# Kernel tuning notes

Measured on AMD Instinct MI355X. Metric: run time of the kernel, lower is better.

## Reference

```python
import jax, jax.numpy as jnp
import numpy as np

B, C, K, N = 16, 512, 64, 8192
STAGE_NUM = 3


def setup_inputs() -> dict:
    key = jax.random.key(0)
    k0, k1, k2, k3 = jax.random.split(key, 4)
    x = jax.random.normal(k0, (B, C, N), jnp.float32)
    # conv1: Conv1d(c, c, 1) with bias; weight init N(0, sqrt(2/c))
    w1 = jax.random.normal(k1, (C, C), jnp.float32) * np.float32(np.sqrt(2.0 / C))
    b1 = jnp.zeros((C,), jnp.float32)
    # conv2: Conv1d(c, c, 1, bias=False) + BatchNorm1d(c) (gamma=1, beta=0)
    w2 = jax.random.normal(k2, (C, C), jnp.float32) * np.float32(np.sqrt(2.0 / C))
    gamma = jnp.ones((C,), jnp.float32)
    beta = jnp.zeros((C,), jnp.float32)
    # mu buffer: (1, c, k), N(0, sqrt(2/k)); is_normalized=False so no l2norm
    mu0 = jax.random.normal(k3, (1, C, K), jnp.float32) * np.float32(np.sqrt(2.0 / K))
    return {"x": x, "w1": w1, "b1": b1, "mu0": mu0, "w2": w2, "gamma": gamma, "beta": beta}


def reference(x, w1, b1, mu0, w2, gamma, beta):
    idn = x                                             # B,C,N
    # conv1 (1x1 conv == per-point matmul)
    x1 = jnp.einsum('oc,bcn->bon', w1, x) + b1[None, :, None]
    # EM iterations run under torch.no_grad() -> stop_gradient
    xs = jax.lax.stop_gradient(x1)
    mu = jnp.broadcast_to(mu0, (x.shape[0], C, K))      # B,C,K (buffer, no grad)
    z = None
    for _ in range(STAGE_NUM):
        z = jax.nn.softmax(jnp.einsum('bcn,bck->bnk', xs, mu), axis=2)  # E-step
        z_ = z / (1e-6 + z.sum(axis=1, keepdims=True))                  # normalize over N
        mu = jnp.einsum('bcn,bnk->bck', xs, z_)                         # M-step
        # is_normalized=False -> _l2norm is identity
    # reconstruction: mu @ z^T, relu
    x2 = jax.nn.relu(jnp.einsum('bck,bnk->bcn', mu, z))
    # conv2 (1x1, no bias) + BatchNorm1d (training-mode batch stats, eps=1e-5)
    x3 = jnp.einsum('oc,bcn->bon', w2, x2)
    mean = x3.mean(axis=(0, 2), keepdims=True)
    var = x3.var(axis=(0, 2), keepdims=True)
    y = gamma[None, :, None] * (x3 - mean) * jax.lax.rsqrt(var + 1e-5) + beta[None, :, None]
    out = y + idn
    return (out, mu)
```

## Files before the change

### kernel.cpp

```cpp
#include <hip/hip_runtime.h>
#include <math.h>

constexpr int B_ = 16, C_ = 512, K_ = 64, N_ = 8192;
constexpr int BHALF = 8;

typedef __bf16 bf16;
typedef __bf16 bf16x4 __attribute__((ext_vector_type(4)));
typedef __bf16 bf16x8 __attribute__((ext_vector_type(8)));
typedef float f32x4 __attribute__((ext_vector_type(4)));

#define GLDS16(gp, lp)                                              \
  __builtin_amdgcn_global_load_lds(                                 \
      (const __attribute__((address_space(1))) unsigned int*)(gp),  \
      (__attribute__((address_space(3))) unsigned int*)(lp), 16, 0, 0)

__device__ __forceinline__ bf16 lo_part(float v, bf16 h) {
  return (bf16)(v - (float)h);
}

__global__ __launch_bounds__(256) void transpose_split_x(
    const float* __restrict__ X, bf16* __restrict__ XTH, bf16* __restrict__ XTL) {
  const int b = blockIdx.z, c0 = blockIdx.y * 64, n0 = blockIdx.x * 64;
  __shared__ float tile[64][65];
  const int tid = threadIdx.x;
  const int rr = tid >> 4, q4 = (tid & 15) << 2;
#pragma unroll
  for (int r = 0; r < 4; ++r) {
    const int c = r * 16 + rr;
    *reinterpret_cast<float4*>(&tile[c][q4]) = *reinterpret_cast<const float4*>(
        &X[((size_t)b * C_ + c0 + c) * N_ + n0 + q4]);
  }
  __syncthreads();
#pragma unroll
  for (int r = 0; r < 4; ++r) {
    const int n = r * 16 + rr;
    bf16x4 oh, ol;
#pragma unroll
    for (int e = 0; e < 4; ++e) {
      const float v = tile[q4 + e][n];
      const bf16 h = (bf16)v;
      oh[e] = h;
      ol[e] = lo_part(v, h);
    }
    const size_t off = ((size_t)b * N_ + n0 + n) * C_ + c0 + q4;
    *reinterpret_cast<bf16x4*>(&XTH[off]) = oh;
    *reinterpret_cast<bf16x4*>(&XTL[off]) = ol;
  }
}

__global__ void cast_w_split(const float* __restrict__ W, bf16* __restrict__ H,
                             bf16* __restrict__ L) {
  const int i = blockIdx.x * 256 + threadIdx.x;
  const float v = W[i];
  const bf16 h = (bf16)v;
  H[i] = h;
  L[i] = lo_part(v, h);
}

__global__ void cast_mu0T_split(const float* __restrict__ MU0,
                                bf16* __restrict__ H, bf16* __restrict__ L) {
  const int k = blockIdx.x;
  for (int c = threadIdx.x; c < C_; c += 256) {
    const float v = MU0[c * K_ + k];
    const bf16 h = (bf16)v;
    H[k * C_ + c] = h;
    L[k * C_ + c] = lo_part(v, h);
  }
}

__global__ __launch_bounds__(256) void conv1_split(
    const bf16* __restrict__ XTH, const bf16* __restrict__ XTL,
    const bf16* __restrict__ W1H, const bf16* __restrict__ W1L,
    const float* __restrict__ bias, bf16* __restrict__ XSH,
    bf16* __restrict__ XSL) {
  const int bz = blockIdx.z;
  const int m0 = blockIdx.x * 128, n0 = blockIdx.y * 128;
  const bf16* __restrict__ AH = XTH + (size_t)bz * N_ * C_;
  const bf16* __restrict__ AL = XTL + (size_t)bz * N_ * C_;

  __shared__ bf16 Ah[128][64], Al[128][64], Bh[128][64], Bl[128][64];

  const int tid = threadIdx.x, wid = tid >> 6, lane = tid & 63;
  const int lc = lane & 15, hi = lane >> 4;
  const int wm = wid >> 1, wn = wid & 1;

  f32x4 acc[4][4] = {};

  for (int k0 = 0; k0 < C_; k0 += 64) {
#pragma unroll
    for (int it = 0; it < 4; ++it) {
      const int chunk = it * 256 + tid;
      const int row = chunk >> 3, k8 = (chunk & 7) << 3;
      const size_t doff = (size_t)(it * 256 + wid * 64) * 8;
      GLDS16(AH + (size_t)(m0 + row) * C_ + k0 + k8, &Ah[0][0] + doff);
      GLDS16(AL + (size_t)(m0 + row) * C_ + k0 + k8, &Al[0][0] + doff);
      GLDS16(W1H + (size_t)(n0 + row) * C_ + k0 + k8, &Bh[0][0] + doff);
      GLDS16(W1L + (size_t)(n0 + row) * C_ + k0 + k8, &Bl[0][0] + doff);
    }
    __syncthreads();
#pragma unroll
    for (int ks = 0; ks < 2; ++ks) {
      bf16x8 ah[4], al4[4], bh[4], bl4[4];
      const int kc = (ks * 4 + hi) * 8;
#pragma unroll
      for (int i = 0; i < 4; ++i) {
        ah[i] = *reinterpret_cast<const bf16x8*>(&Ah[wm * 64 + i * 16 + lc][kc]);
        al4[i] = *reinterpret_cast<const bf16x8*>(&Al[wm * 64 + i * 16 + lc][kc]);
      }
#pragma unroll
      for (int j = 0; j < 4; ++j) {
        bh[j] = *reinterpret_cast<const bf16x8*>(&Bh[wn * 64 + j * 16 + lc][kc]);
        bl4[j] = *reinterpret_cast<const bf16x8*>(&Bl[wn * 64 + j * 16 + lc][kc]);
      }
#pragma unroll
      for (int i = 0; i < 4; ++i)
#pragma unroll
        for (int j = 0; j < 4; ++j) {
          acc[i][j] = __builtin_amdgcn_mfma_f32_16x16x32_bf16(al4[i], bh[j], acc[i][j], 0, 0, 0);
          acc[i][j] = __builtin_amdgcn_mfma_f32_16x16x32_bf16(ah[i], bl4[j], acc[i][j], 0, 0, 0);
          acc[i][j] = __builtin_amdgcn_mfma_f32_16x16x32_bf16(ah[i], bh[j], acc[i][j], 0, 0, 0);
        }
    }
    __syncthreads();
  }

#pragma unroll
  for (int j = 0; j < 4; ++j) {
    const int col = n0 + wn * 64 + j * 16 + lc;
    const float bv = bias[col];
#pragma unroll
    for (int i = 0; i < 4; ++i) {
      const int row0 = m0 + wm * 64 + i * 16 + hi * 4;
#pragma unroll
      for (int r = 0; r < 4; ++r) {
        const float v = acc[i][j][r] + bv;
        const size_t off = ((size_t)bz * N_ + row0 + r) * C_ + col;
        const bf16 h = (bf16)v;
        XSH[off] = h;
        XSL[off] = lo_part(v, h);
      }
    }
  }
}

__global__ __launch_bounds__(256) void estep_split(
    const bf16* __restrict__ XSH, const bf16* __restrict__ XSL,
    const bf16* __restrict__ MTH, const bf16* __restrict__ MTL,
    size_t mustride, bf16* __restrict__ ZH, bf16* __restrict__ ZL,
    float* __restrict__ colsum) {
  const int b = blockIdx.y;
  const int m0 = blockIdx.x * 128;
  const bf16* __restrict__ AHp = XSH + (size_t)b * N_ * C_;
  const bf16* __restrict__ ALp = XSL + (size_t)b * N_ * C_;
  const bf16* __restrict__ BHp = MTH + (size_t)b * mustride;
  const bf16* __restrict__ BLp = MTL + (size_t)b * mustride;

  __shared__ bf16 Ah[128][64], Al[128][64], Bh[64][64], Bl[64][64];
  __shared__ float cs[64];

  const int tid = threadIdx.x, wid = tid >> 6, lane = tid & 63;
  const int lc = lane & 15, hi = lane >> 4;
  if (tid < 64) cs[tid] = 0.0f;

  f32x4 acc[2][4] = {};
  for (int k0 = 0; k0 < C_; k0 += 64) {
#pragma unroll
    for (int it = 0; it < 4; ++it) {
      const int chunk = it * 256 + tid;
      const int row = chunk >> 3, k8 = (chunk & 7) << 3;
      const size_t doff = (size_t)(it * 256 + wid * 64) * 8;
      GLDS16(AHp + (size_t)(m0 + row) * C_ + k0 + k8, &Ah[0][0] + doff);
      GLDS16(ALp + (size_t)(m0 + row) * C_ + k0 + k8, &Al[0][0] + doff);
    }
#pragma unroll
    for (int it = 0; it < 2; ++it) {
      const int chunk = it * 256 + tid;
      const int row = chunk >> 3, k8 = (chunk & 7) << 3;
      const size_t doff = (size_t)(it * 256 + wid * 64) * 8;
      GLDS16(BHp + (size_t)row * C_ + k0 + k8, &Bh[0][0] + doff);
      GLDS16(BLp + (size_t)row * C_ + k0 + k8, &Bl[0][0] + doff);
    }
    __syncthreads();
#pragma unroll
    for (int ks = 0; ks < 2; ++ks) {
      const int kc = (ks * 4 + hi) * 8;
      bf16x8 ah[2], al4[2], bh[4], bl4[4];
#pragma unroll
      for (int i = 0; i < 2; ++i) {
        ah[i] = *reinterpret_cast<const bf16x8*>(&Ah[wid * 32 + i * 16 + lc][kc]);
        al4[i] = *reinterpret_cast<const bf16x8*>(&Al[wid * 32 + i * 16 + lc][kc]);
      }
#pragma unroll
      for (int j = 0; j < 4; ++j) {
        bh[j] = *reinterpret_cast<const bf16x8*>(&Bh[j * 16 + lc][kc]);
        bl4[j] = *reinterpret_cast<const bf16x8*>(&Bl[j * 16 + lc][kc]);
      }
#pragma unroll
      for (int i = 0; i < 2; ++i)
#pragma unroll
        for (int j = 0; j < 4; ++j) {
          acc[i][j] = __builtin_amdgcn_mfma_f32_16x16x32_bf16(al4[i], bh[j], acc[i][j], 0, 0, 0);
          acc[i][j] = __builtin_amdgcn_mfma_f32_16x16x32_bf16(ah[i], bl4[j], acc[i][j], 0, 0, 0);
          acc[i][j] = __builtin_amdgcn_mfma_f32_16x16x32_bf16(ah[i], bh[j], acc[i][j], 0, 0, 0);
        }
    }
    __syncthreads();
  }

  float cp[4] = {0.f, 0.f, 0.f, 0.f};
#pragma unroll
  for (int i = 0; i < 2; ++i) {
#pragma unroll
    for (int r = 0; r < 4; ++r) {
      float v0 = acc[i][0][r], v1 = acc[i][1][r], v2 = acc[i][2][r], v3 = acc[i][3][r];
      float mx = fmaxf(fmaxf(v0, v1), fmaxf(v2, v3));
#pragma unroll
      for (int off = 1; off < 16; off <<= 1) mx = fmaxf(mx, __shfl_xor(mx, off));
      float p0 = __expf(v0 - mx), p1 = __expf(v1 - mx);
      float p2 = __expf(v2 - mx), p3 = __expf(v3 - mx);
      float s = p0 + p1 + p2 + p3;
#pragma unroll
      for (int off = 1; off < 16; off <<= 1) s += __shfl_xor(s, off);
      const float inv = 1.0f / s;
      p0 *= inv; p1 *= inv; p2 *= inv; p3 *= inv;
      const int n = m0 + wid * 32 + i * 16 + hi * 4 + r;
      bf16* zh = ZH + ((size_t)b * N_ + n) * K_;
      bf16* zl = ZL + ((size_t)b * N_ + n) * K_;
      const float pv[4] = {p0, p1, p2, p3};
#pragma unroll
      for (int j = 0; j < 4; ++j) {
        const bf16 h = (bf16)pv[j];
        zh[j * 16 + lc] = h;
        zl[j * 16 + lc] = lo_part(pv[j], h);
        cp[j] += pv[j];
      }
    }
  }
#pragma unroll
  for (int j = 0; j < 4; ++j) atomicAdd(&cs[j * 16 + lc], cp[j]);
  __syncthreads();
  if (tid < 64) atomicAdd(&colsum[b * K_ + tid], cs[tid]);
}

__global__ __launch_bounds__(128) void mstep_split(
    const bf16* __restrict__ XSH, const bf16* __restrict__ XSL,
    const bf16* __restrict__ ZHp, const bf16* __restrict__ ZLp,
    float* __restrict__ MUACC) {
  const int b = blockIdx.z;
  const int c0 = blockIdx.y * 128;
  const int nbase = blockIdx.x * 1024;
  const bf16* __restrict__ XbH = XSH + (size_t)b * N_ * C_;
  const bf16* __restrict__ XbL = XSL + (size_t)b * N_ * C_;
  const bf16* __restrict__ ZbH = ZHp + (size_t)b * N_ * K_;
  const bf16* __restrict__ ZbL = ZLp + (size_t)b * N_ * K_;

  __shared__ bf16 Ah[128][32], Al[128][32], Bh[64][32], Bl[64][32];

  const int tid = threadIdx.x, wid = tid >> 6, lane = tid & 63;
  const int lc = lane & 15, hi = lane >> 4;

  f32x4 acc[4][4] = {};
  for (int n0 = nbase; n0 < nbase + 1024; n0 += 32) {
#pragma unroll
    for (int it = 0; it < 4; ++it) {
      const int chunk = it * 128 + tid;
      const int nn = chunk & 31, c8 = (chunk >> 5) * 8;
      const bf16x8 vh = *reinterpret_cast<const bf16x8*>(
          &XbH[(size_t)(n0 + nn) * C_ + c0 + c8]);
      const bf16x8 vl = *reinterpret_cast<const bf16x8*>(
          &XbL[(size_t)(n0 + nn) * C_ + c0 + c8]);
#pragma unroll
      for (int e = 0; e < 8; ++e) {
        Ah[c8 + e][nn] = vh[e];
        Al[c8 + e][nn] = vl[e];
      }
    }
#pragma unroll
    for (int it = 0; it < 2; ++it) {
      const int chunk = it * 128 + tid;
      const int nn = chunk & 31, k8 = (chunk >> 5) * 8;
      const bf16x8 vh = *reinterpret_cast<const bf16x8*>(
          &ZbH[(size_t)(n0 + nn) * K_ + k8]);
      const bf16x8 vl = *reinterpret_cast<const bf16x8*>(
          &ZbL[(size_t)(n0 + nn) * K_ + k8]);
#pragma unroll
      for (int e = 0; e < 8; ++e) {
        Bh[k8 + e][nn] = vh[e];
        Bl[k8 + e][nn] = vl[e];
      }
    }
    __syncthreads();
    bf16x8 ah[4], al4[4], bh[4], bl4[4];
#pragma unroll
    for (int i = 0; i < 4; ++i) {
      ah[i] = *reinterpret_cast<const bf16x8*>(&Ah[wid * 64 + i * 16 + lc][hi * 8]);
      al4[i] = *reinterpret_cast<const bf16x8*>(&Al[wid * 64 + i * 16 + lc][hi * 8]);
    }
#pragma unroll
    for (int j = 0; j < 4; ++j) {
      bh[j] = *reinterpret_cast<const bf16x8*>(&Bh[j * 16 + lc][hi * 8]);
      bl4[j] = *reinterpret_cast<const bf16x8*>(&Bl[j * 16 + lc][hi * 8]);
    }
#pragma unroll
    for (int i = 0; i < 4; ++i)
#pragma unroll
      for (int j = 0; j < 4; ++j) {
        acc[i][j] = __builtin_amdgcn_mfma_f32_16x16x32_bf16(al4[i], bh[j], acc[i][j], 0, 0, 0);
        acc[i][j] = __builtin_amdgcn_mfma_f32_16x16x32_bf16(ah[i], bl4[j], acc[i][j], 0, 0, 0);
        acc[i][j] = __builtin_amdgcn_mfma_f32_16x16x32_bf16(ah[i], bh[j], acc[i][j], 0, 0, 0);
      }
    __syncthreads();
  }
#pragma unroll
  for (int i = 0; i < 4; ++i) {
    const int c = c0 + wid * 64 + i * 16 + hi * 4;
#pragma unroll
    for (int r = 0; r < 4; ++r)
#pragma unroll
      for (int j = 0; j < 4; ++j)
        atomicAdd(&MUACC[((size_t)b * C_ + c + r) * K_ + j * 16 + lc], acc[i][j][r]);
  }
}

__global__ void finalize_mu(const float* __restrict__ MUACC,
                            const float* __restrict__ colsum,
                            bf16* __restrict__ MUTH, bf16* __restrict__ MUTL,
                            bf16* __restrict__ MUH, float* __restrict__ muout) {
  const int idx = blockIdx.x * 256 + threadIdx.x;
  const int k = idx & (K_ - 1);
  const int c = (idx >> 6) & (C_ - 1);
  const int b = idx >> 15;
  const float v = MUACC[idx] / (1e-6f + colsum[b * K_ + k]);
  const bf16 h = (bf16)v;
  MUH[idx] = h;
  MUTH[((size_t)b * K_ + k) * C_ + c] = h;
  MUTL[((size_t)b * K_ + k) * C_ + c] = lo_part(v, h);
  if (muout) muout[idx] = v;
}

__global__ __launch_bounds__(256) void x2_plain(
    const bf16* __restrict__ ZHp, const bf16* __restrict__ MUHp,
    bf16* __restrict__ X2) {
  const int b = blockIdx.z;
  const int m0 = blockIdx.x * 128, n0 = blockIdx.y * 128;
  const bf16* __restrict__ Ab = ZHp + (size_t)b * N_ * K_;
  const bf16* __restrict__ Bb = MUHp + (size_t)b * C_ * K_;

  __shared__ bf16 As[128][64], Bs[128][64];

  const int tid = threadIdx.x, wid = tid >> 6, lane = tid & 63;
  const int lc = lane & 15, hi = lane >> 4;
  const int wm = wid >> 1, wn = wid & 1;

  f32x4 acc[4][4] = {};
#pragma unroll
  for (int it = 0; it < 4; ++it) {
    const int chunk = it * 256 + tid;
    const int row = chunk >> 3, k8 = (chunk & 7) << 3;
    const size_t doff = (size_t)(it * 256 + wid * 64) * 8;
    GLDS16(Ab + (size_t)(m0 + row) * K_ + k8, &As[0][0] + doff);
    GLDS16(Bb + (size_t)(n0 + row) * K_ + k8, &Bs[0][0] + doff);
  }
  __syncthreads();
#pragma unroll
  for (int ks = 0; ks < 2; ++ks) {
    const int kc = (ks * 4 + hi) * 8;
    bf16x8 af[4], bg[4];
#pragma unroll
    for (int i = 0; i < 4; ++i)
      af[i] = *reinterpret_cast<const bf16x8*>(&As[wm * 64 + i * 16 + lc][kc]);
#pragma unroll
    for (int j = 0; j < 4; ++j)
      bg[j] = *reinterpret_cast<const bf16x8*>(&Bs[wn * 64 + j * 16 + lc][kc]);
#pragma unroll
    for (int i = 0; i < 4; ++i)
#pragma unroll
      for (int j = 0; j < 4; ++j)
        acc[i][j] = __builtin_amdgcn_mfma_f32_16x16x32_bf16(af[i], bg[j], acc[i][j], 0, 0, 0);
  }

#pragma unroll
  for (int j = 0; j < 4; ++j) {
    const int col = n0 + wn * 64 + j * 16 + lc;
#pragma unroll
    for (int i = 0; i < 4; ++i) {
      const int row0 = m0 + wm * 64 + i * 16 + hi * 4;
#pragma unroll
      for (int r = 0; r < 4; ++r)
        X2[((size_t)b * N_ + row0 + r) * C_ + col] = (bf16)fmaxf(acc[i][j][r], 0.0f);
    }
  }
}

__global__ __launch_bounds__(256) void conv2_plain(
    const bf16* __restrict__ W2H, const bf16* __restrict__ X2,
    float* __restrict__ OUT) {
  const int b = blockIdx.z;
  const int m0 = blockIdx.x * 128, n0 = blockIdx.y * 128;
  const bf16* __restrict__ Bb = X2 + (size_t)b * N_ * C_;

  __shared__ bf16 As[128][64], Bs[128][64];

  const int tid = threadIdx.x, wid = tid >> 6, lane = tid & 63;
  const int lc = lane & 15, hi = lane >> 4;
  const int wm = wid >> 1, wn = wid & 1;

  f32x4 acc[4][4] = {};
  for (int k0 = 0; k0 < C_; k0 += 64) {
#pragma unroll
    for (int it = 0; it < 4; ++it) {
      const int chunk = it * 256 + tid;
      const int row = chunk >> 3, k8 = (chunk & 7) << 3;
      const size_t doff = (size_t)(it * 256 + wid * 64) * 8;
      GLDS16(W2H + (size_t)(m0 + row) * C_ + k0 + k8, &As[0][0] + doff);
      GLDS16(Bb + (size_t)(n0 + row) * C_ + k0 + k8, &Bs[0][0] + doff);
    }
    __syncthreads();
#pragma unroll
    for (int ks = 0; ks < 2; ++ks) {
      const int kc = (ks * 4 + hi) * 8;
      bf16x8 af[4], bg[4];
#pragma unroll
      for (int i = 0; i < 4; ++i)
        af[i] = *reinterpret_cast<const bf16x8*>(&As[wm * 64 + i * 16 + lc][kc]);
#pragma unroll
      for (int j = 0; j < 4; ++j)
        bg[j] = *reinterpret_cast<const bf16x8*>(&Bs[wn * 64 + j * 16 + lc][kc]);
#pragma unroll
      for (int i = 0; i < 4; ++i)
#pragma unroll
        for (int j = 0; j < 4; ++j)
          acc[i][j] = __builtin_amdgcn_mfma_f32_16x16x32_bf16(af[i], bg[j], acc[i][j], 0, 0, 0);
    }
    __syncthreads();
  }

#pragma unroll
  for (int j = 0; j < 4; ++j) {
    const int col = n0 + wn * 64 + j * 16 + lc;
#pragma unroll
    for (int i = 0; i < 4; ++i) {
      const int row0 = m0 + wm * 64 + i * 16 + hi * 4;
#pragma unroll
      for (int r = 0; r < 4; ++r)
        OUT[((size_t)b * C_ + row0 + r) * N_ + col] = acc[i][j][r];
    }
  }
}

__global__ __launch_bounds__(256) void bn_stats_kernel(
    const float* __restrict__ X3, float* __restrict__ meanp, float* __restrict__ rstdp) {
  const int c = blockIdx.x;
  const int tid = threadIdx.x;
  double s = 0.0, s2 = 0.0;
  for (int b = 0; b < B_; ++b) {
    const float4* p = reinterpret_cast<const float4*>(X3 + ((size_t)b * C_ + c) * N_);
    for (int i = tid; i < N_ / 4; i += 256) {
      const float4 v = p[i];
      s += (double)v.x + (double)v.y + (double)v.z + (double)v.w;
      s2 += (double)v.x * v.x + (double)v.y * v.y + (double)v.z * v.z + (double)v.w * v.w;
    }
  }
  __shared__ double sh[256];
  __shared__ double sh2[256];
  sh[tid] = s; sh2[tid] = s2;
  __syncthreads();
  for (int off = 128; off > 0; off >>= 1) {
    if (tid < off) { sh[tid] += sh[tid + off]; sh2[tid] += sh2[tid + off]; }
    __syncthreads();
  }
  if (tid == 0) {
    const double inv = 1.0 / ((double)B_ * N_);
    const double m = sh[0] * inv;
    const double var = sh2[0] * inv - m * m;
    meanp[c] = (float)m;
    rstdp[c] = (float)rsqrt(var + 1e-5);
  }
}

__global__ __launch_bounds__(256) void bn_apply_kernel(
    float* __restrict__ OUT, const float* __restrict__ Xin,
    const float* __restrict__ gamma, const float* __restrict__ beta,
    const float* __restrict__ meanp, const float* __restrict__ rstdp) {
  const size_t total4 = (size_t)B_ * C_ * N_ / 4;
  for (size_t i = (size_t)blockIdx.x * 256 + threadIdx.x; i < total4;
       i += (size_t)gridDim.x * 256) {
    const int c = (int)((i >> 11) & (C_ - 1));
    const float g = gamma[c] * rstdp[c];
    const float o = beta[c] - meanp[c] * g;
    float4 v = reinterpret_cast<const float4*>(OUT)[i];
    const float4 xi = reinterpret_cast<const float4*>(Xin)[i];
    v.x = v.x * g + o + xi.x;
    v.y = v.y * g + o + xi.y;
    v.z = v.z * g + o + xi.z;
    v.w = v.w * g + o + xi.w;
    reinterpret_cast<float4*>(OUT)[i] = v;
  }
}

extern "C" void kernel_launch(void* const* d_in, const int* in_sizes, int n_in,
                              void* d_out, int out_size, void* d_ws,
                              size_t ws_size, hipStream_t stream) {
  (void)in_sizes; (void)n_in; (void)out_size; (void)ws_size;
  const float* x     = (const float*)d_in[0];
  const float* w1    = (const float*)d_in[1];
  const float* b1    = (const float*)d_in[2];
  const float* mu0   = (const float*)d_in[3];
  const float* w2    = (const float*)d_in[4];
  const float* gamma = (const float*)d_in[5];
  const float* beta  = (const float*)d_in[6];

  bf16* XSH = (bf16*)d_out;
  bf16* XSL = XSH + (size_t)B_ * N_ * C_;
  float* OUT = (float*)d_out;
  float* MUOUT = OUT + (size_t)B_ * C_ * N_;

  bf16* XTH = (bf16*)d_ws;
  bf16* XTL = XTH + (size_t)BHALF * N_ * C_;
  bf16* X2b = XTH;
  bf16* ZH  = XTH + (size_t)B_ * N_ * C_;
  bf16* ZL  = ZH + (size_t)B_ * N_ * K_;
  bf16* W1H = ZL + (size_t)B_ * N_ * K_;
  bf16* W1L = W1H + C_ * C_;
  bf16* W2H = W1L + C_ * C_;
  bf16* W2L = W2H + C_ * C_;
  bf16* MT0H = W2L + C_ * C_;
  bf16* MT0L = MT0H + K_ * C_;
  bf16* MUTH = MT0L + K_ * C_;
  bf16* MUTL = MUTH + (size_t)B_ * K_ * C_;
  bf16* MUH  = MUTL + (size_t)B_ * K_ * C_;
  float* MUACC = (float*)(MUH + (size_t)B_ * C_ * K_);
  float* colsum = MUACC + (size_t)B_ * C_ * K_;
  float* meanp = colsum + B_ * K_;
  float* rstdp = meanp + C_;

  const dim3 blk(256);

  cast_w_split<<<dim3(C_ * C_ / 256), blk, 0, stream>>>(w1, W1H, W1L);
  cast_w_split<<<dim3(C_ * C_ / 256), blk, 0, stream>>>(w2, W2H, W2L);
  cast_mu0T_split<<<dim3(K_), blk, 0, stream>>>(mu0, MT0H, MT0L);

  for (int half = 0; half < 2; ++half) {
    const float* xh = x + (size_t)half * BHALF * C_ * N_;
    transpose_split_x<<<dim3(N_ / 64, C_ / 64, BHALF), blk, 0, stream>>>(xh, XTH, XTL);
    conv1_split<<<dim3(N_ / 128, C_ / 128, BHALF), blk, 0, stream>>>(
        XTH, XTL, W1H, W1L, b1,
        XSH + (size_t)half * BHALF * N_ * C_, XSL + (size_t)half * BHALF * N_ * C_);
  }

  for (int it = 0; it < 3; ++it) {
    hipMemsetAsync(colsum, 0, B_ * K_ * sizeof(float), stream);
    estep_split<<<dim3(N_ / 128, B_), blk, 0, stream>>>(
        XSH, XSL, it == 0 ? MT0H : MUTH, it == 0 ? MT0L : MUTL,
        it == 0 ? 0 : (size_t)K_ * C_, ZH, ZL, colsum);
    hipMemsetAsync(MUACC, 0, (size_t)B_ * C_ * K_ * sizeof(float), stream);
    mstep_split<<<dim3(N_ / 1024, C_ / 128, B_), dim3(128), 0, stream>>>(
        XSH, XSL, ZH, ZL, MUACC);
    finalize_mu<<<dim3(B_ * C_ * K_ / 256), blk, 0, stream>>>(
        MUACC, colsum, MUTH, MUTL, MUH, it == 2 ? MUOUT : nullptr);
  }

  x2_plain<<<dim3(N_ / 128, C_ / 128, B_), blk, 0, stream>>>(ZH, MUH, X2b);
  conv2_plain<<<dim3(C_ / 128, N_ / 128, B_), blk, 0, stream>>>(W2H, X2b, OUT);
  bn_stats_kernel<<<dim3(C_), blk, 0, stream>>>(OUT, meanp, rstdp);
  bn_apply_kernel<<<dim3(2048), blk, 0, stream>>>(OUT, x, gamma, beta, meanp, rstdp);
}
```

Before: 1.304 ms.

## Swizzle LDS tiles, fuse BN stats into conv2, regroup EM by batch

Applies an XOR swizzle to LDS tile columns in conv1, estep, x2 and conv2 to avoid bank conflicts, and pads the mstep LDS tiles. The BN statistics pass is fused into the conv2 epilogue through shuffle reductions and float atomics, with a small finalize kernel, which removes a full re-read of the output. The EM loop now runs in two batch groups so each group's XS working set may stay cache-resident, and the mstep N-chunk is halved for more parallelism. The float32 sum and sum-of-squares accumulation replaces the double-precision statistics and may lose precision in the variance.

New measurement: 1.386 ms. 1.06x slower.

```diff
diff --git a/kernel.cpp b/kernel.cpp
--- a/kernel.cpp
+++ b/kernel.cpp
@@ -3,6 +3,8 @@
 
 constexpr int B_ = 16, C_ = 512, K_ = 64, N_ = 8192;
 constexpr int BHALF = 8;
+constexpr int BGRP = 8;
+constexpr int MCHUNK = 512;
 
 typedef __bf16 bf16;
 typedef __bf16 bf16x4 __attribute__((ext_vector_type(4)));
@@ -83,6 +85,7 @@
   const int tid = threadIdx.x, wid = tid >> 6, lane = tid & 63;
   const int lc = lane & 15, hi = lane >> 4;
   const int wm = wid >> 1, wn = wid & 1;
+  const int swz = lc & 7;
 
   f32x4 acc[4][4] = {};
 
@@ -90,18 +93,19 @@
 #pragma unroll
     for (int it = 0; it < 4; ++it) {
       const int chunk = it * 256 + tid;
-      const int row = chunk >> 3, k8 = (chunk & 7) << 3;
+      const int row = chunk >> 3;
+      const int koff = (((chunk & 7) ^ (row & 7)) << 3);
       const size_t doff = (size_t)(it * 256 + wid * 64) * 8;
-      GLDS16(AH + (size_t)(m0 + row) * C_ + k0 + k8, &Ah[0][0] + doff);
-      GLDS16(AL + (size_t)(m0 + row) * C_ + k0 + k8, &Al[0][0] + doff);
-      GLDS16(W1H + (size_t)(n0 + row) * C_ + k0 + k8, &Bh[0][0] + doff);
-      GLDS16(W1L + (size_t)(n0 + row) * C_ + k0 + k8, &Bl[0][0] + doff);
+      GLDS16(AH + (size_t)(m0 + row) * C_ + k0 + koff, &Ah[0][0] + doff);
+      GLDS16(AL + (size_t)(m0 + row) * C_ + k0 + koff, &Al[0][0] + doff);
+      GLDS16(W1H + (size_t)(n0 + row) * C_ + k0 + koff, &Bh[0][0] + doff);
+      GLDS16(W1L + (size_t)(n0 + row) * C_ + k0 + koff, &Bl[0][0] + doff);
     }
     __syncthreads();
 #pragma unroll
     for (int ks = 0; ks < 2; ++ks) {
       bf16x8 ah[4], al4[4], bh[4], bl4[4];
-      const int kc = (ks * 4 + hi) * 8;
+      const int kc = (((ks << 2) + hi) ^ swz) << 3;
 #pragma unroll
       for (int i = 0; i < 4; ++i) {
         ah[i] = *reinterpret_cast<const bf16x8*>(&Ah[wm * 64 + i * 16 + lc][kc]);
@@ -147,8 +151,8 @@
     const bf16* __restrict__ XSH, const bf16* __restrict__ XSL,
     const bf16* __restrict__ MTH, const bf16* __restrict__ MTL,
     size_t mustride, bf16* __restrict__ ZH, bf16* __restrict__ ZL,
-    float* __restrict__ colsum) {
-  const int b = blockIdx.y;
+    float* __restrict__ colsum, int b_base) {
+  const int b = b_base + blockIdx.y;
   const int m0 = blockIdx.x * 128;
   const bf16* __restrict__ AHp = XSH + (size_t)b * N_ * C_;
   const bf16* __restrict__ ALp = XSL + (size_t)b * N_ * C_;
@@ -160,6 +164,7 @@
 
   const int tid = threadIdx.x, wid = tid >> 6, lane = tid & 63;
   const int lc = lane & 15, hi = lane >> 4;
+  const int swz = lc & 7;
   if (tid < 64) cs[tid] = 0.0f;
 
   f32x4 acc[2][4] = {};
@@ -167,23 +172,25 @@
 #pragma unroll
     for (int it = 0; it < 4; ++it) {
       const int chunk = it * 256 + tid;
-      const int row = chunk >> 3, k8 = (chunk & 7) << 3;
+      const int row = chunk >> 3;
+      const int koff = (((chunk & 7) ^ (row & 7)) << 3);
       const size_t doff = (size_t)(it * 256 + wid * 64) * 8;
-      GLDS16(AHp + (size_t)(m0 + row) * C_ + k0 + k8, &Ah[0][0] + doff);
-      GLDS16(ALp + (size_t)(m0 + row) * C_ + k0 + k8, &Al[0][0] + doff);
+      GLDS16(AHp + (size_t)(m0 + row) * C_ + k0 + koff, &Ah[0][0] + doff);
+      GLDS16(ALp + (size_t)(m0 + row) * C_ + k0 + koff, &Al[0][0] + doff);
     }
 #pragma unroll
     for (int it = 0; it < 2; ++it) {
       const int chunk = it * 256 + tid;
-      const int row = chunk >> 3, k8 = (chunk & 7) << 3;
+      const int row = chunk >> 3;
+      const int koff = (((chunk & 7) ^ (row & 7)) << 3);
       const size_t doff = (size_t)(it * 256 + wid * 64) * 8;
-      GLDS16(BHp + (size_t)row * C_ + k0 + k8, &Bh[0][0] + doff);
-      GLDS16(BLp + (size_t)row * C_ + k0 + k8, &Bl[0][0] + doff);
+      GLDS16(BHp + (size_t)row * C_ + k0 + koff, &Bh[0][0] + doff);
+      GLDS16(BLp + (size_t)row * C_ + k0 + koff, &Bl[0][0] + doff);
     }
     __syncthreads();
 #pragma unroll
     for (int ks = 0; ks < 2; ++ks) {
-      const int kc = (ks * 4 + hi) * 8;
+      const int kc = (((ks << 2) + hi) ^ swz) << 3;
       bf16x8 ah[2], al4[2], bh[4], bl4[4];
 #pragma unroll
       for (int i = 0; i < 2; ++i) {
@@ -245,22 +252,22 @@
 __global__ __launch_bounds__(128) void mstep_split(
     const bf16* __restrict__ XSH, const bf16* __restrict__ XSL,
     const bf16* __restrict__ ZHp, const bf16* __restrict__ ZLp,
-    float* __restrict__ MUACC) {
-  const int b = blockIdx.z;
+    float* __restrict__ MUACC, int b_base) {
+  const int b = b_base + blockIdx.z;
   const int c0 = blockIdx.y * 128;
-  const int nbase = blockIdx.x * 1024;
+  const int nbase = blockIdx.x * MCHUNK;
   const bf16* __restrict__ XbH = XSH + (size_t)b * N_ * C_;
   const bf16* __restrict__ XbL = XSL + (size_t)b * N_ * C_;
   const bf16* __restrict__ ZbH = ZHp + (size_t)b * N_ * K_;
   const bf16* __restrict__ ZbL = ZLp + (size_t)b * N_ * K_;
 
-  __shared__ bf16 Ah[128][32], Al[128][32], Bh[64][32], Bl[64][32];
+  __shared__ bf16 Ah[128][40], Al[128][40], Bh[64][40], Bl[64][40];
 
   const int tid = threadIdx.x, wid = tid >> 6, lane = tid & 63;
   const int lc = lane & 15, hi = lane >> 4;
 
   f32x4 acc[4][4] = {};
-  for (int n0 = nbase; n0 < nbase + 1024; n0 += 32) {
+  for (int n0 = nbase; n0 < nbase + MCHUNK; n0 += 32) {
 #pragma unroll
     for (int it = 0; it < 4; ++it) {
       const int chunk = it * 128 + tid;
@@ -325,8 +332,9 @@
 __global__ void finalize_mu(const float* __restrict__ MUACC,
                             const float* __restrict__ colsum,
                             bf16* __restrict__ MUTH, bf16* __restrict__ MUTL,
-                            bf16* __restrict__ MUH, float* __restrict__ muout) {
-  const int idx = blockIdx.x * 256 + threadIdx.x;
+                            bf16* __restrict__ MUH, float* __restrict__ muout,
+                            int idx_base) {
+  const int idx = idx_base + blockIdx.x * 256 + threadIdx.x;
   const int k = idx & (K_ - 1);
   const int c = (idx >> 6) & (C_ - 1);
   const int b = idx >> 15;
@@ -351,20 +359,22 @@
   const int tid = threadIdx.x, wid = tid >> 6, lane = tid & 63;
   const int lc = lane & 15, hi = lane >> 4;
   const int wm = wid >> 1, wn = wid & 1;
+  const int swz = lc & 7;
 
   f32x4 acc[4][4] = {};
 #pragma unroll
   for (int it = 0; it < 4; ++it) {
     const int chunk = it * 256 + tid;
-    const int row = chunk >> 3, k8 = (chunk & 7) << 3;
+    const int row = chunk >> 3;
+    const int koff = (((chunk & 7) ^ (row & 7)) << 3);
     const size_t doff = (size_t)(it * 256 + wid * 64) * 8;
-    GLDS16(Ab + (size_t)(m0 + row) * K_ + k8, &As[0][0] + doff);
-    GLDS16(Bb + (size_t)(n0 + row) * K_ + k8, &Bs[0][0] + doff);
+    GLDS16(Ab + (size_t)(m0 + row) * K_ + koff, &As[0][0] + doff);
+    GLDS16(Bb + (size_t)(n0 + row) * K_ + koff, &Bs[0][0] + doff);
   }
   __syncthreads();
 #pragma unroll
   for (int ks = 0; ks < 2; ++ks) {
-    const int kc = (ks * 4 + hi) * 8;
+    const int kc = (((ks << 2) + hi) ^ swz) << 3;
     bf16x8 af[4], bg[4];
 #pragma unroll
     for (int i = 0; i < 4; ++i)
@@ -394,7 +404,8 @@
 
 __global__ __launch_bounds__(256) void conv2_plain(
     const bf16* __restrict__ W2H, const bf16* __restrict__ X2,
-    float* __restrict__ OUT) {
+    float* __restrict__ OUT, float* __restrict__ bnsum,
+    float* __restrict__ bnsq) {
   const int b = blockIdx.z;
   const int m0 = blockIdx.x * 128, n0 = blockIdx.y * 128;
   const bf16* __restrict__ Bb = X2 + (size_t)b * N_ * C_;
@@ -404,21 +415,23 @@
   const int tid = threadIdx.x, wid = tid >> 6, lane = tid & 63;
   const int lc = lane & 15, hi = lane >> 4;
   const int wm = wid >> 1, wn = wid & 1;
+  const int swz = lc & 7;
 
   f32x4 acc[4][4] = {};
   for (int k0 = 0; k0 < C_; k0 += 64) {
 #pragma unroll
     for (int it = 0; it < 4; ++it) {
       const int chunk = it * 256 + tid;
-      const int row = chunk >> 3, k8 = (chunk & 7) << 3;
+      const int row = chunk >> 3;
+      const int koff = (((chunk & 7) ^ (row & 7)) << 3);
       const size_t doff = (size_t)(it * 256 + wid * 64) * 8;
-      GLDS16(W2H + (size_t)(m0 + row) * C_ + k0 + k8, &As[0][0] + doff);
-      GLDS16(Bb + (size_t)(n0 + row) * C_ + k0 + k8, &Bs[0][0] + doff);
+      GLDS16(W2H + (size_t)(m0 + row) * C_ + k0 + koff, &As[0][0] + doff);
+      GLDS16(Bb + (size_t)(n0 + row) * C_ + k0 + koff, &Bs[0][0] + doff);
     }
     __syncthreads();
 #pragma unroll
     for (int ks = 0; ks < 2; ++ks) {
-      const int kc = (ks * 4 + hi) * 8;
+      const int kc = (((ks << 2) + hi) ^ swz) << 3;
       bf16x8 af[4], bg[4];
 #pragma unroll
       for (int i = 0; i < 4; ++i)
@@ -435,6 +448,8 @@
     __syncthreads();
   }
 
+  float psum[4][4] = {};
+  float psq[4][4] = {};
 #pragma unroll
   for (int j = 0; j < 4; ++j) {
     const int col = n0 + wn * 64 + j * 16 + lc;
@@ -442,40 +457,47 @@
     for (int i = 0; i < 4; ++i) {
       const int row0 = m0 + wm * 64 + i * 16 + hi * 4;
 #pragma unroll
-      for (int r = 0; r < 4; ++r)
-        OUT[((size_t)b * C_ + row0 + r) * N_ + col] = acc[i][j][r];
-    }
-  }
-}
-
-__global__ __launch_bounds__(256) void bn_stats_kernel(
-    const float* __restrict__ X3, float* __restrict__ meanp, float* __restrict__ rstdp) {
-  const int c = blockIdx.x;
-  const int tid = threadIdx.x;
-  double s = 0.0, s2 = 0.0;
-  for (int b = 0; b < B_; ++b) {
-    const float4* p = reinterpret_cast<const float4*>(X3 + ((size_t)b * C_ + c) * N_);
-    for (int i = tid; i < N_ / 4; i += 256) {
-      const float4 v = p[i];
-      s += (double)v.x + (double)v.y + (double)v.z + (double)v.w;
-      s2 += (double)v.x * v.x + (double)v.y * v.y + (double)v.z * v.z + (double)v.w * v.w;
-    }
-  }
-  __shared__ double sh[256];
-  __shared__ double sh2[256];
-  sh[tid] = s; sh2[tid] = s2;
-  __syncthreads();
-  for (int off = 128; off > 0; off >>= 1) {
-    if (tid < off) { sh[tid] += sh[tid + off]; sh2[tid] += sh2[tid + off]; }
-    __syncthreads();
-  }
-  if (tid == 0) {
-    const double inv = 1.0 / ((double)B_ * N_);
-    const double m = sh[0] * inv;
-    const double var = sh2[0] * inv - m * m;
-    meanp[c] = (float)m;
-    rstdp[c] = (float)rsqrt(var + 1e-5);
-  }
+      for (int r = 0; r < 4; ++r) {
+        const float v = acc[i][j][r];
+        OUT[((size_t)b * C_ + row0 + r) * N_ + col] = v;
+        psum[i][r] += v;
+        psq[i][r] += v * v;
+      }
+    }
+  }
+#pragma unroll
+  for (int off = 1; off < 16; off <<= 1) {
+#pragma unroll
+    for (int i = 0; i < 4; ++i)
+#pragma unroll
+      for (int r = 0; r < 4; ++r) {
+        psum[i][r] += __shfl_xor(psum[i][r], off);
+        psq[i][r] += __shfl_xor(psq[i][r], off);
+      }
+  }
+  if (lc == 0) {
+#pragma unroll
+    for (int i = 0; i < 4; ++i) {
+      const int ch = m0 + wm * 64 + i * 16 + hi * 4;
+#pragma unroll
+      for (int r = 0; r < 4; ++r) {
+        atomicAdd(&bnsum[ch + r], psum[i][r]);
+        atomicAdd(&bnsq[ch + r], psq[i][r]);
+      }
+    }
+  }
+}
+
+__global__ void bn_finalize(const float* __restrict__ bnsum,
+                            const float* __restrict__ bnsq,
+                            float* __restrict__ meanp, float* __restrict__ rstdp) {
+  const int c = blockIdx.x * 256 + threadIdx.x;
+  if (c >= C_) return;
+  const float inv = 1.0f / ((float)B_ * N_);
+  const float m = bnsum[c] * inv;
+  const float var = bnsq[c] * inv - m * m;
+  meanp[c] = m;
+  rstdp[c] = rsqrtf(var + 1e-5f);
 }
 
 __global__ __launch_bounds__(256) void bn_apply_kernel(
@@ -533,6 +555,8 @@
   float* colsum = MUACC + (size_t)B_ * C_ * K_;
   float* meanp = colsum + B_ * K_;
   float* rstdp = meanp + C_;
+  float* bnsum = rstdp + C_;
+  float* bnsq  = bnsum + C_;
 
   const dim3 blk(256);
 
@@ -548,20 +572,27 @@
         XSH + (size_t)half * BHALF * N_ * C_, XSL + (size_t)half * BHALF * N_ * C_);
   }
 
-  for (int it = 0; it < 3; ++it) {
-    hipMemsetAsync(colsum, 0, B_ * K_ * sizeof(float), stream);
-    estep_split<<<dim3(N_ / 128, B_), blk, 0, stream>>>(
-        XSH, XSL, it == 0 ? MT0H : MUTH, it == 0 ? MT0L : MUTL,
-        it == 0 ? 0 : (size_t)K_ * C_, ZH, ZL, colsum);
-    hipMemsetAsync(MUACC, 0, (size_t)B_ * C_ * K_ * sizeof(float), stream);
-    mstep_split<<<dim3(N_ / 1024, C_ / 128, B_), dim3(128), 0, stream>>>(
-        XSH, XSL, ZH, ZL, MUACC);
-    finalize_mu<<<dim3(B_ * C_ * K_ / 256), blk, 0, stream>>>(
-        MUACC, colsum, MUTH, MUTL, MUH, it == 2 ? MUOUT : nullptr);
+  for (int g = 0; g < B_ / BGRP; ++g) {
+    const int boff = g * BGRP;
+    for (int it = 0; it < 3; ++it) {
+      hipMemsetAsync(colsum + boff * K_, 0, BGRP * K_ * sizeof(float), stream);
+      estep_split<<<dim3(N_ / 128, BGRP), blk, 0, stream>>>(
+          XSH, XSL, it == 0 ? MT0H : MUTH, it == 0 ? MT0L : MUTL,
+          it == 0 ? 0 : (size_t)K_ * C_, ZH, ZL, colsum, boff);
+      hipMemsetAsync(MUACC + (size_t)boff * C_ * K_, 0,
+                     (size_t)BGRP * C_ * K_ * sizeof(float), stream);
+      mstep_split<<<dim3(N_ / MCHUNK, C_ / 128, BGRP), dim3(128), 0, stream>>>(
+          XSH, XSL, ZH, ZL, MUACC, boff);
+      finalize_mu<<<dim3(BGRP * C_ * K_ / 256), blk, 0, stream>>>(
+          MUACC, colsum, MUTH, MUTL, MUH, it == 2 ? MUOUT : nullptr,
+          boff * C_ * K_);
+    }
   }
 
   x2_plain<<<dim3(N_ / 128, C_ / 128, B_), blk, 0, stream>>>(ZH, MUH, X2b);
-  conv2_plain<<<dim3(C_ / 128, N_ / 128, B_), blk, 0, stream>>>(W2H, X2b, OUT);
-  bn_stats_kernel<<<dim3(C_), blk, 0, stream>>>(OUT, meanp, rstdp);
+  hipMemsetAsync(bnsum, 0, 2 * C_ * sizeof(float), stream);
+  conv2_plain<<<dim3(C_ / 128, N_ / 128, B_), blk, 0, stream>>>(
+      W2H, X2b, OUT, bnsum, bnsq);
+  bn_finalize<<<dim3(2), blk, 0, stream>>>(bnsum, bnsq, meanp, rstdp);
   bn_apply_kernel<<<dim3(2048), blk, 0, stream>>>(OUT, x, gamma, beta, meanp, rstdp);
 }
```
